# Kernel optimization log

Measured on AMD Instinct MI355X. Metric: run time of the kernel, lower is better.

The kernel has to match this reference:

```python
import jax, jax.numpy as jnp
import numpy as np

B, L, C = 4, 4096, 1024
NH, CS = 16, 16
HF = C // NH            # 64
NC = L // CS            # 256
LR = 1.0


def setup_inputs() -> dict:
    key = jax.random.key(0)
    ks = jax.random.split(key, 9)
    s = 0.02
    return {
        "hidden_states": jax.random.normal(ks[0], (B, L, C), jnp.float32),
        "Wq": jax.random.normal(ks[1], (C, C), jnp.float32) * s,
        "Wk": jax.random.normal(ks[2], (C, C), jnp.float32) * s,
        "Wv": jax.random.normal(ks[3], (C, C), jnp.float32) * s,
        "Wo": jax.random.normal(ks[4], (C, C), jnp.float32) * s,
        "ilr_w": jax.random.normal(ks[5], (C, NH), jnp.float32) * s,
        "ilr_b": jnp.zeros((NH,), jnp.float32),
        "W1": jax.random.normal(ks[6], (NH, HF, 4 * HF), jnp.float32) * s,
        "W2": jax.random.normal(ks[7], (NH, 4 * HF, HF), jnp.float32) * s,
    }


def _split(x):
    # [B,L,C] -> [B,NH,NC,CS,HF]
    return x.reshape(B, NC, CS, NH, HF).transpose(0, 3, 1, 2, 4)


def reference(hidden_states, Wq, Wk, Wv, Wo, ilr_w, ilr_b, W1, W2):
    XC = _split(hidden_states @ Wq)
    XB = _split(hidden_states @ Wk)
    XA = _split(hidden_states @ Wv)

    # inner-loop learning rate: [B,NH,NC,CS,1]
    ilr = jax.nn.sigmoid(hidden_states.reshape(B, NC, CS, C) @ ilr_w + ilr_b)
    ilr = ilr.transpose(0, 3, 1, 2)[..., None]
    token_idx = 1.0 / jnp.arange(1, CS + 1, dtype=jnp.float32)
    coeff = (LR * token_idx).reshape(1, 1, 1, CS, 1) * ilr / HF

    tril = jnp.tril(jnp.ones((CS, CS), hidden_states.dtype))

    # per-(batch,head) inner states
    W1s = jnp.broadcast_to(W1[None], (B, NH, HF, 4 * HF))
    W2s = jnp.broadcast_to(W2[None], (B, NH, 4 * HF, HF))

    def step(carry, xs):
        W1_s, W2_s = carry
        XA_c, XB_c, XC_c, coeff_c = xs          # [B,NH,CS,HF], coeff [B,NH,CS,1]
        coeff_last = coeff_c[..., -1:, :]        # [B,NH,1,1]
        Z1 = XB_c @ W1_s                         # [B,NH,CS,4HF]
        Z2 = Z1 @ W2_s                           # [B,NH,CS,HF]
        g2 = Z2 - XA_c
        g1 = g2 @ jnp.swapaxes(W2_s, -1, -2)
        Attn1 = tril * (XC_c @ jnp.swapaxes(XB_c, -1, -2))
        Z1_bar = XC_c @ W1_s - coeff_c * (Attn1 @ g1)
        W1_s = W1_s - jnp.swapaxes(coeff_last * XB_c, -1, -2) @ g1
        Attn2 = tril * (Z1_bar @ jnp.swapaxes(Z1, -1, -2))
        Z2_bar = Z1_bar @ W2_s - coeff_c * (Attn2 @ g2)
        W2_s = W2_s - jnp.swapaxes(coeff_last * Z1, -1, -2) @ g2
        return (W1_s, W2_s), Z2_bar

    # move chunk axis to front for scan: [NC,B,NH,CS,*]
    xs = tuple(t.transpose(2, 0, 1, 3, 4) for t in (XA, XB, XC, coeff))
    _, Z2_bars = jax.lax.scan(step, (W1s, W2s), xs)

    # [NC,B,NH,CS,HF] -> [B,NC,CS,NH,HF] -> [B,L,C]
    out = Z2_bars.transpose(1, 0, 3, 2, 4).reshape(B, L, C)
    return out @ Wo
```

## Files before the change

kernel.cpp:

```cpp
#include <hip/hip_runtime.h>

#define Bsz  4
#define Lsz  4096
#define Csz  1024
#define NHsz 16
#define CSsz 16
#define HFsz 64
#define HF4sz 256
#define NCsz 256

typedef __attribute__((ext_vector_type(8))) short  bhalf8;
typedef __attribute__((ext_vector_type(4))) float  floatx4;

__device__ __forceinline__ unsigned short bf_rne(float x) {
  const unsigned u = __float_as_uint(x);
  return (unsigned short)((u + 0x7fffu + ((u >> 16) & 1u)) >> 16);
}
__device__ __forceinline__ void split_rne(float x, unsigned short& h, unsigned short& l) {
  h = bf_rne(x);
  const float hf = __uint_as_float((unsigned)h << 16);
  l = bf_rne(x - hf);
}

__global__ __launch_bounds__(256)
void split32(const float* __restrict__ in, unsigned short* __restrict__ hi,
             unsigned short* __restrict__ lo)
{
  const int i = (blockIdx.x * 256 + threadIdx.x) * 4;
  const float4 v = *(const float4*)&in[i];
  ushort4 h, l;
  split_rne(v.x, h.x, l.x);
  split_rne(v.y, h.y, l.y);
  split_rne(v.z, h.z, l.z);
  split_rne(v.w, h.w, l.w);
  *(ushort4*)&hi[i] = h;
  *(ushort4*)&lo[i] = l;
}

__global__ __launch_bounds__(256)
void gemm_mfma(const unsigned short* __restrict__ Ahi,
               const unsigned short* __restrict__ Alo,
               const float* __restrict__ Bm,
               float* __restrict__ Cm, int M, int N, int K)
{
  __shared__ unsigned short sAh[128 * 40];
  __shared__ unsigned short sAl[128 * 40];
  __shared__ unsigned short sBh[128 * 40];
  __shared__ unsigned short sBl[128 * 40];

  const int t    = threadIdx.x;
  const int lane = t & 63, w = t >> 6;
  const int wr   = (w >> 1) * 64, wc = (w & 1) * 64;
  const int row0 = blockIdx.y * 128, col0 = blockIdx.x * 128;
  const int fr   = lane & 15, fk = (lane >> 4) * 8;

  floatx4 acc[4][4];
#pragma unroll
  for (int mi = 0; mi < 4; ++mi)
#pragma unroll
    for (int ni = 0; ni < 4; ++ni) acc[mi][ni] = (floatx4){0.f, 0.f, 0.f, 0.f};

  const int arow = t >> 1, akg = (t & 1) * 16;
  const int bc4  = (t & 31) * 4, bk4 = (t >> 5) * 4;

  for (int k0 = 0; k0 < K; k0 += 32) {
    {
      const size_t ga = (size_t)(row0 + arow) * K + k0 + akg;
      const bhalf8 h0 = *(const bhalf8*)&Ahi[ga];
      const bhalf8 h1 = *(const bhalf8*)&Ahi[ga + 8];
      const bhalf8 l0 = *(const bhalf8*)&Alo[ga];
      const bhalf8 l1 = *(const bhalf8*)&Alo[ga + 8];
      *(bhalf8*)&sAh[arow * 40 + akg]     = h0;
      *(bhalf8*)&sAh[arow * 40 + akg + 8] = h1;
      *(bhalf8*)&sAl[arow * 40 + akg]     = l0;
      *(bhalf8*)&sAl[arow * 40 + akg + 8] = l1;
    }
    {
      const float4 r0 = *(const float4*)&Bm[(size_t)(k0 + bk4 + 0) * N + col0 + bc4];
      const float4 r1 = *(const float4*)&Bm[(size_t)(k0 + bk4 + 1) * N + col0 + bc4];
      const float4 r2 = *(const float4*)&Bm[(size_t)(k0 + bk4 + 2) * N + col0 + bc4];
      const float4 r3 = *(const float4*)&Bm[(size_t)(k0 + bk4 + 3) * N + col0 + bc4];
#define STORE_BCOL(v0, v1, v2, v3, c) do {                                   \
      unsigned short h0_, h1_, h2_, h3_, l0_, l1_, l2_, l3_;                 \
      split_rne(v0, h0_, l0_); split_rne(v1, h1_, l1_);                      \
      split_rne(v2, h2_, l2_); split_rne(v3, h3_, l3_);                      \
      const int off_ = (bc4 + (c)) * 40 + bk4;                               \
      *(unsigned*)&sBh[off_]     = (unsigned)h0_ | ((unsigned)h1_ << 16);    \
      *(unsigned*)&sBh[off_ + 2] = (unsigned)h2_ | ((unsigned)h3_ << 16);    \
      *(unsigned*)&sBl[off_]     = (unsigned)l0_ | ((unsigned)l1_ << 16);    \
      *(unsigned*)&sBl[off_ + 2] = (unsigned)l2_ | ((unsigned)l3_ << 16);    \
    } while (0)
      STORE_BCOL(r0.x, r1.x, r2.x, r3.x, 0);
      STORE_BCOL(r0.y, r1.y, r2.y, r3.y, 1);
      STORE_BCOL(r0.z, r1.z, r2.z, r3.z, 2);
      STORE_BCOL(r0.w, r1.w, r2.w, r3.w, 3);
#undef STORE_BCOL
    }
    __syncthreads();

    bhalf8 ah[4], al[4];
#pragma unroll
    for (int mi = 0; mi < 4; ++mi) {
      ah[mi] = *(const bhalf8*)&sAh[(wr + mi * 16 + fr) * 40 + fk];
      al[mi] = *(const bhalf8*)&sAl[(wr + mi * 16 + fr) * 40 + fk];
    }
#pragma unroll
    for (int ni = 0; ni < 4; ++ni) {
      const bhalf8 bh = *(const bhalf8*)&sBh[(wc + ni * 16 + fr) * 40 + fk];
      const bhalf8 bl = *(const bhalf8*)&sBl[(wc + ni * 16 + fr) * 40 + fk];
#pragma unroll
      for (int mi = 0; mi < 4; ++mi) {
        acc[mi][ni] = __builtin_amdgcn_mfma_f32_16x16x32_bf16(ah[mi], bh, acc[mi][ni], 0, 0, 0);
        acc[mi][ni] = __builtin_amdgcn_mfma_f32_16x16x32_bf16(ah[mi], bl, acc[mi][ni], 0, 0, 0);
        acc[mi][ni] = __builtin_amdgcn_mfma_f32_16x16x32_bf16(al[mi], bh, acc[mi][ni], 0, 0, 0);
      }
    }
    __syncthreads();
  }

  const int er = (lane >> 4) * 4;
#pragma unroll
  for (int mi = 0; mi < 4; ++mi)
#pragma unroll
    for (int ni = 0; ni < 4; ++ni) {
      const size_t base = (size_t)(row0 + wr + mi * 16 + er) * N + col0 + wc + ni * 16 + fr;
#pragma unroll
      for (int j = 0; j < 4; ++j)
        Cm[base + (size_t)j * N] = acc[mi][ni][j];
    }
}

__global__ __launch_bounds__(256)
void ilr_coeff(const float* __restrict__ H, const float* __restrict__ Wil,
               const float* __restrict__ bil, float* __restrict__ coeff)
{
  __shared__ float sRow[4][1024];
  __shared__ float sP[4][16][17];
  const int t = threadIdx.x;
  const size_t r0 = (size_t)blockIdx.x * 4;
  for (int rr = 0; rr < 4; ++rr)
    for (int c = t; c < 1024; c += 256)
      sRow[rr][c] = H[(r0 + rr) * 1024 + c];
  __syncthreads();
  const int hh = t & 15, sl = t >> 4;
  for (int rr = 0; rr < 4; ++rr) {
    float acc = 0.f;
    for (int kk = 0; kk < 64; ++kk)
      acc += sRow[rr][sl * 64 + kk] * Wil[(sl * 64 + kk) * 16 + hh];
    sP[rr][sl][hh] = acc;
  }
  __syncthreads();
  if (t < 64) {
    const int rr = t >> 4, h2 = t & 15;
    float s = 0.f;
    for (int sl2 = 0; sl2 < 16; ++sl2) s += sP[rr][sl2][h2];
    s += bil[h2];
    const float sig = 1.f / (1.f + expf(-s));
    const int r  = (int)(r0 + rr);
    const int b  = r >> 12, l = r & 4095, nc = l >> 4, cs = l & 15;
    coeff[((b * 16 + h2) * NCsz + nc) * CSsz + cs] = sig / ((float)(cs + 1) * 64.0f);
  }
}

__global__ __launch_bounds__(512) __attribute__((amdgpu_waves_per_eu(1, 2)))
void ttt_scan(const float* __restrict__ XA, const float* __restrict__ XBuf,
              const float* __restrict__ XCbuf, const float* __restrict__ coeff,
              const float* __restrict__ W1g, const float* __restrict__ W2g,
              float* __restrict__ Out)
{
  __shared__ __attribute__((aligned(16))) float sg2[16 * 68];
  __shared__ __attribute__((aligned(16))) float sZ1[16 * 260];
  __shared__ __attribute__((aligned(16))) float sZ1b[16 * 260];
  __shared__ __attribute__((aligned(16))) float sTmp[10624];
  __shared__ float sA1[16 * 17];
  __shared__ float sA2[16 * 17];
  __shared__ float sCoBuf[2 * 16];

  const int t   = threadIdx.x;
  const int bh  = blockIdx.x;
  const int b   = bh >> 4, h = bh & 15;
  const bool isA = (t < 256);
  const int n   = t & 255;
  const int m   = t & 63, q = (t >> 6) & 3;

  float wreg[128];
#define W1R(k)  wreg[(k)]
#define ZBR(i)  wreg[64 + (i)]
#define G1R(i)  wreg[80 + (i)]
#define W2RR(k) wreg[(k)]
#define W2CR(k) wreg[64 + (k)]

  float xa0, xa1;

  const float* W1h = W1g + h * HFsz * HF4sz;
  const float* W2h = W2g + h * HF4sz * HFsz;
  if (isA) {
#pragma unroll
    for (int k = 0; k < 64; ++k) W1R(k) = W1h[k * 256 + n];
  } else {
#pragma unroll
    for (int mm = 0; mm < 64; ++mm) W2RR(mm) = W2h[n * 64 + mm];
#pragma unroll
    for (int kk = 0; kk < 64; ++kk) W2CR(kk) = W2h[(q * 64 + kk) * 64 + m];
  }

  {
    const int cb0 = (b * Lsz) * Csz + h * HFsz;
    if (t < 16) sCoBuf[t] = coeff[(bh * NCsz + 0) * CSsz + t];
    const int ibr = t >> 6, mm = t & 63;
    xa0 = XA[cb0 + ibr * 1024 + mm];
    xa1 = XA[cb0 + (ibr + 8) * 1024 + mm];
  }
  __syncthreads();

#pragma unroll 1
  for (int nc = 0; nc < NCsz; ++nc) {
    const int cur = nc & 1, nxt = cur ^ 1;
    const int cb  = (b * Lsz + nc * CSsz) * Csz + h * HFsz;
    const int nc1 = (nc + 1) & (NCsz - 1);
    const int cb1 = (b * Lsz + nc1 * CSsz) * Csz + h * HFsz;
    const float* __restrict__ xbG = XBuf  + cb;
    const float* __restrict__ xcG = XCbuf + cb;

    const float cl = sCoBuf[cur * 16 + 15];
    float conext = 0.f;
    if (isA && t < 16) conext = coeff[(bh * NCsz + nc1) * CSsz + t];

    if (isA) {
      float acc[16];
#pragma unroll
      for (int i = 0; i < 16; ++i) {
        float a0 = 0.f, a1 = 0.f;
#pragma unroll
        for (int k = 0; k < 64; k += 8) {
          const float4 x0 = *(const float4*)&xbG[i * 1024 + k];
          const float4 x1 = *(const float4*)&xbG[i * 1024 + k + 4];
          a0 = fmaf(x0.w, W1R(k + 3), fmaf(x0.z, W1R(k + 2),
               fmaf(x0.y, W1R(k + 1), fmaf(x0.x, W1R(k), a0))));
          a1 = fmaf(x1.w, W1R(k + 7), fmaf(x1.z, W1R(k + 6),
               fmaf(x1.y, W1R(k + 5), fmaf(x1.x, W1R(k + 4), a1))));
        }
        acc[i] = a0 + a1;
      }
#pragma unroll
      for (int i = 0; i < 16; ++i) sZ1[i * 260 + n] = acc[i];
    } else {
      const int ia = n >> 4, ja = n & 15;
      float a0 = 0.f, a1 = 0.f;
      if (ja <= ia) {
#pragma unroll
        for (int k = 0; k < 64; k += 8) {
          const float4 c0 = *(const float4*)&xcG[ia * 1024 + k];
          const float4 b0 = *(const float4*)&xbG[ja * 1024 + k];
          const float4 c1 = *(const float4*)&xcG[ia * 1024 + k + 4];
          const float4 b1 = *(const float4*)&xbG[ja * 1024 + k + 4];
          a0 = fmaf(c0.w, b0.w, fmaf(c0.z, b0.z, fmaf(c0.y, b0.y, fmaf(c0.x, b0.x, a0))));
          a1 = fmaf(c1.w, b1.w, fmaf(c1.z, b1.z, fmaf(c1.y, b1.y, fmaf(c1.x, b1.x, a1))));
        }
      }
      sA1[ia * 17 + ja] = a0 + a1;
    }
    __syncthreads();

    if (isA) {
#pragma unroll
      for (int i = 0; i < 16; ++i) {
        float a0 = 0.f, a1 = 0.f;
#pragma unroll
        for (int k = 0; k < 64; k += 8) {
          const float4 x0 = *(const float4*)&xcG[i * 1024 + k];
          const float4 x1 = *(const float4*)&xcG[i * 1024 + k + 4];
          a0 = fmaf(x0.w, W1R(k + 3), fmaf(x0.z, W1R(k + 2),
               fmaf(x0.y, W1R(k + 1), fmaf(x0.x, W1R(k), a0))));
          a1 = fmaf(x1.w, W1R(k + 7), fmaf(x1.z, W1R(k + 6),
               fmaf(x1.y, W1R(k + 5), fmaf(x1.x, W1R(k + 4), a1))));
        }
        ZBR(i) = a0 + a1;
      }
    } else {
      const int qo = q << 6;
      float acc[16];
#pragma unroll
      for (int i = 0; i < 16; ++i) acc[i] = 0.f;
#pragma unroll
      for (int kk = 0; kk < 64; kk += 4) {
        const float wa = W2CR(kk), wb = W2CR(kk + 1), wc = W2CR(kk + 2), wd = W2CR(kk + 3);
#pragma unroll
        for (int i = 0; i < 16; ++i) {
          const float4 z = *(const float4*)&sZ1[i * 260 + qo + kk];
          acc[i] = fmaf(z.w, wd, fmaf(z.z, wc, fmaf(z.y, wb, fmaf(z.x, wa, acc[i]))));
        }
      }
#pragma unroll
      for (int i = 0; i < 16; ++i) sTmp[(q << 10) + (i << 6) + m] = acc[i];
    }
    __syncthreads();

    {
      const int ibr = t >> 6, mm = t & 63;
      const int i1 = ibr + 8;
      float v0 = sTmp[ibr * 64 + mm] + sTmp[1024 + ibr * 64 + mm]
               + sTmp[2048 + ibr * 64 + mm] + sTmp[3072 + ibr * 64 + mm] - xa0;
      float v1 = sTmp[i1 * 64 + mm] + sTmp[1024 + i1 * 64 + mm]
               + sTmp[2048 + i1 * 64 + mm] + sTmp[3072 + i1 * 64 + mm] - xa1;
      sg2[ibr * 68 + mm] = v0;
      sg2[i1 * 68 + mm]  = v1;
      xa0 = XA[cb1 + ibr * 1024 + mm];
      xa1 = XA[cb1 + i1 * 1024 + mm];
      if (t < 16) sCoBuf[nxt * 16 + t] = conext;
    }
    __syncthreads();

    if (!isA) {
      float s[16];
#pragma unroll
      for (int i = 0; i < 16; ++i) s[i] = cl * sZ1[i * 260 + n];
      float acc[16];
#pragma unroll
      for (int i = 0; i < 16; ++i) acc[i] = 0.f;
#pragma unroll
      for (int mm = 0; mm < 64; mm += 4) {
        const float wa = W2RR(mm), wb = W2RR(mm + 1), wc = W2RR(mm + 2), wd = W2RR(mm + 3);
        float d0 = 0.f, d1 = 0.f, d2 = 0.f, d3 = 0.f;
#pragma unroll
        for (int i = 0; i < 16; ++i) {
          const float4 g = *(const float4*)&sg2[i * 68 + mm];
          acc[i] = fmaf(g.w, wd, fmaf(g.z, wc, fmaf(g.y, wb, fmaf(g.x, wa, acc[i]))));
          d0 = fmaf(s[i], g.x, d0); d1 = fmaf(s[i], g.y, d1);
          d2 = fmaf(s[i], g.z, d2); d3 = fmaf(s[i], g.w, d3);
        }
        W2RR(mm + 0) -= d0; W2RR(mm + 1) -= d1; W2RR(mm + 2) -= d2; W2RR(mm + 3) -= d3;
      }
#pragma unroll
      for (int i = 0; i < 16; ++i) sTmp[i * 256 + n] = acc[i];
    }
    __syncthreads();

    if (isA) {
#pragma unroll
      for (int j = 0; j < 16; ++j) G1R(j) = sTmp[j * 256 + n];
#pragma unroll
      for (int i = 0; i < 16; ++i) {
        float at = 0.f;
#pragma unroll
        for (int j = 0; j <= i; ++j) at = fmaf(sA1[i * 17 + j], G1R(j), at);
        ZBR(i) = fmaf(-sCoBuf[cur * 16 + i], at, ZBR(i));
        sZ1b[i * 260 + n] = ZBR(i);
      }
    }
    __syncthreads();

    if (isA) {
      const int ia = n >> 4, ja = n & 15;
      float a0 = 0.f, a1 = 0.f, a2 = 0.f, a3 = 0.f;
      if (ja <= ia) {
#pragma unroll
        for (int kk = 0; kk < 256; kk += 16) {
          const float4 p0 = *(const float4*)&sZ1b[ia * 260 + kk];
          const float4 z0 = *(const float4*)&sZ1 [ja * 260 + kk];
          const float4 p1 = *(const float4*)&sZ1b[ia * 260 + kk + 4];
          const float4 z1 = *(const float4*)&sZ1 [ja * 260 + kk + 4];
          const float4 p2 = *(const float4*)&sZ1b[ia * 260 + kk + 8];
          const float4 z2 = *(const float4*)&sZ1 [ja * 260 + kk + 8];
          const float4 p3 = *(const float4*)&sZ1b[ia * 260 + kk + 12];
          const float4 z3 = *(const float4*)&sZ1 [ja * 260 + kk + 12];
          a0 = fmaf(p0.w, z0.w, fmaf(p0.z, z0.z, fmaf(p0.y, z0.y, fmaf(p0.x, z0.x, a0))));
          a1 = fmaf(p1.w, z1.w, fmaf(p1.z, z1.z, fmaf(p1.y, z1.y, fmaf(p1.x, z1.x, a1))));
          a2 = fmaf(p2.w, z2.w, fmaf(p2.z, z2.z, fmaf(p2.y, z2.y, fmaf(p2.x, z2.x, a2))));
          a3 = fmaf(p3.w, z3.w, fmaf(p3.z, z3.z, fmaf(p3.y, z3.y, fmaf(p3.x, z3.x, a3))));
        }
      }
      sA2[ia * 17 + ja] = (a0 + a1) + (a2 + a3);
#pragma unroll
      for (int i = 0; i < 16; ++i) {
        const float gi = cl * G1R(i);
#pragma unroll
        for (int k = 0; k < 64; k += 4) {
          const float4 x = *(const float4*)&xbG[i * 1024 + k];
          W1R(k + 0) -= gi * x.x; W1R(k + 1) -= gi * x.y;
          W1R(k + 2) -= gi * x.z; W1R(k + 3) -= gi * x.w;
        }
      }
    } else {
      const int qo = q << 6;
      float acc[16];
#pragma unroll
      for (int i = 0; i < 16; ++i) acc[i] = 0.f;
#pragma unroll
      for (int kk = 0; kk < 64; kk += 4) {
        const float wa = W2CR(kk), wb = W2CR(kk + 1), wc = W2CR(kk + 2), wd = W2CR(kk + 3);
#pragma unroll
        for (int i = 0; i < 16; ++i) {
          const float4 z = *(const float4*)&sZ1b[i * 260 + qo + kk];
          acc[i] = fmaf(z.w, wd, fmaf(z.z, wc, fmaf(z.y, wb, fmaf(z.x, wa, acc[i]))));
        }
      }
#pragma unroll
      for (int i = 0; i < 16; ++i) sTmp[(q << 10) + (i << 6) + m] = acc[i];
      float s2[16];
#pragma unroll
      for (int i = 0; i < 16; ++i) s2[i] = cl * sg2[i * 68 + m];
#pragma unroll
      for (int kk = 0; kk < 64; kk += 4) {
        float d0 = 0.f, d1 = 0.f, d2 = 0.f, d3 = 0.f;
#pragma unroll
        for (int i = 0; i < 16; ++i) {
          const float4 z = *(const float4*)&sZ1[i * 260 + qo + kk];
          d0 = fmaf(s2[i], z.x, d0); d1 = fmaf(s2[i], z.y, d1);
          d2 = fmaf(s2[i], z.z, d2); d3 = fmaf(s2[i], z.w, d3);
        }
        W2CR(kk + 0) -= d0; W2CR(kk + 1) -= d1; W2CR(kk + 2) -= d2; W2CR(kk + 3) -= d3;
      }
    }
    __syncthreads();

    if (isA) {
      const int q4 = n >> 6, mm = n & 63;
#pragma unroll
      for (int r = 0; r < 4; ++r) {
        const int i = q4 + 4 * r;
        float v = sTmp[i * 64 + mm] + sTmp[1024 + i * 64 + mm]
                + sTmp[2048 + i * 64 + mm] + sTmp[3072 + i * 64 + mm];
        float at = 0.f;
#pragma unroll
        for (int j = 0; j < 16; ++j) at = fmaf(sA2[i * 17 + j], sg2[j * 68 + mm], at);
        Out[cb + i * 1024 + mm] = v - sCoBuf[cur * 16 + i] * at;
      }
    }
  }
#undef W1R
#undef ZBR
#undef G1R
#undef W2RR
#undef W2CR
}

extern "C" void kernel_launch(void* const* d_in, const int* in_sizes, int n_in,
                              void* d_out, int out_size, void* d_ws, size_t ws_size,
                              hipStream_t stream)
{
  const float* H    = (const float*)d_in[0];
  const float* Wq   = (const float*)d_in[1];
  const float* Wk   = (const float*)d_in[2];
  const float* Wv   = (const float*)d_in[3];
  const float* Wo   = (const float*)d_in[4];
  const float* Wil  = (const float*)d_in[5];
  const float* bil  = (const float*)d_in[6];
  const float* W1   = (const float*)d_in[7];
  const float* W2   = (const float*)d_in[8];
  float* out        = (float*)d_out;

  float* ws    = (float*)d_ws;
  float* bXC   = ws;
  float* bXB   = ws + 16777216;
  float* bZ2b  = ws + 33554432;
  float* bCo   = ws + 50331648;
  float* bXA   = out;

  unsigned short* hHi = (unsigned short*)bZ2b;
  unsigned short* hLo = hHi + 16777216;
  unsigned short* zHi = (unsigned short*)bXC;
  unsigned short* zLo = zHi + 16777216;

  const int M = Bsz * Lsz, N = Csz, K = Csz;
  dim3 gm(N / 128, M / 128);
  dim3 bm(256);

  split32<<<16384, 256, 0, stream>>>(H, hHi, hLo);
  gemm_mfma<<<gm, bm, 0, stream>>>(hHi, hLo, Wq, bXC, M, N, K);
  gemm_mfma<<<gm, bm, 0, stream>>>(hHi, hLo, Wk, bXB, M, N, K);
  gemm_mfma<<<gm, bm, 0, stream>>>(hHi, hLo, Wv, bXA, M, N, K);
  ilr_coeff<<<M / 4, 256, 0, stream>>>(H, Wil, bil, bCo);
  ttt_scan<<<Bsz * NHsz, 512, 0, stream>>>(bXA, bXB, bXC, bCo, W1, W2, bZ2b);
  split32<<<16384, 256, 0, stream>>>(bZ2b, zHi, zLo);
  gemm_mfma<<<gm, bm, 0, stream>>>(zHi, zLo, Wo, out, M, N, K);
}
```

Measured before the change: 9.513 ms.

## Move TTT scan chunk matmuls onto bf16x3 MFMA with split-precision fragments

Rewrites the per-chunk inner loop of the sequential TTT scan so the Z1, XC·W1, Z2, g1, Z2_bar and Attn2 products run on 16x16x32 bf16 MFMA instructions. Each fp32 operand is split into hi/lo bf16 parts and three MFMAs per tile approximate fp32 accuracy. Register and shared-memory layouts are reorganised around MFMA fragments: W2 is mirrored into shared memory as hi/lo bf16, transposed copies of Z1, G1 and XB support the weight updates, and the pipeline gains extra barriers. The scalar FMA work and LDS traffic of the old VALU path should shrink, at the cost of split/convert overhead, a slightly different numerical result, and more synchronisation steps per chunk.

```diff
diff --git a/kernel.cpp b/kernel.cpp
--- a/kernel.cpp
+++ b/kernel.cpp
@@ -21,6 +21,29 @@
   const float hf = __uint_as_float((unsigned)h << 16);
   l = bf_rne(x - hf);
 }
+__device__ __forceinline__ void tsplit(float x, unsigned short& h, unsigned short& l) {
+  const unsigned u = __float_as_uint(x);
+  h = (unsigned short)(u >> 16);
+  const float r = x - __uint_as_float(u & 0xffff0000u);
+  l = bf_rne(r);
+}
+__device__ __forceinline__ void split_frag8(const float* __restrict__ x,
+                                            bhalf8& h, bhalf8& l) {
+#pragma unroll
+  for (int e = 0; e < 8; ++e) {
+    unsigned short hs, ls;
+    tsplit(x[e], hs, ls);
+    h[e] = (short)hs; l[e] = (short)ls;
+  }
+}
+__device__ __forceinline__ float recon2(unsigned short h, unsigned short l) {
+  return __uint_as_float((unsigned)h << 16) + __uint_as_float((unsigned)l << 16);
+}
+
+#define MFMA3(acc, ah, al, bh, bl)                                            \
+  acc = __builtin_amdgcn_mfma_f32_16x16x32_bf16(ah, bh, acc, 0, 0, 0);        \
+  acc = __builtin_amdgcn_mfma_f32_16x16x32_bf16(ah, bl, acc, 0, 0, 0);        \
+  acc = __builtin_amdgcn_mfma_f32_16x16x32_bf16(al, bh, acc, 0, 0, 0);
 
 __global__ __launch_bounds__(256)
 void split32(const float* __restrict__ in, unsigned short* __restrict__ hi,
@@ -162,90 +185,138 @@
   }
 }
 
-__global__ __launch_bounds__(512) __attribute__((amdgpu_waves_per_eu(1, 2)))
+__global__ __launch_bounds__(512)
 void ttt_scan(const float* __restrict__ XA, const float* __restrict__ XBuf,
               const float* __restrict__ XCbuf, const float* __restrict__ coeff,
               const float* __restrict__ W1g, const float* __restrict__ W2g,
               float* __restrict__ Out)
 {
-  __shared__ __attribute__((aligned(16))) float sg2[16 * 68];
-  __shared__ __attribute__((aligned(16))) float sZ1[16 * 260];
-  __shared__ __attribute__((aligned(16))) float sZ1b[16 * 260];
-  __shared__ __attribute__((aligned(16))) float sTmp[10624];
-  __shared__ float sA1[16 * 17];
-  __shared__ float sA2[16 * 17];
-  __shared__ float sCoBuf[2 * 16];
-
-  const int t   = threadIdx.x;
-  const int bh  = blockIdx.x;
-  const int b   = bh >> 4, h = bh & 15;
-  const bool isA = (t < 256);
-  const int n   = t & 255;
-  const int m   = t & 63, q = (t >> 6) & 3;
-
-  float wreg[128];
-#define W1R(k)  wreg[(k)]
-#define ZBR(i)  wreg[64 + (i)]
-#define G1R(i)  wreg[80 + (i)]
-#define W2RR(k) wreg[(k)]
-#define W2CR(k) wreg[64 + (k)]
-
-  float xa0, xa1;
+  __shared__ __attribute__((aligned(16))) unsigned short sW2h[256 * 72];
+  __shared__ __attribute__((aligned(16))) unsigned short sW2l[256 * 72];
+  __shared__ __attribute__((aligned(16))) unsigned short sZ1h[16 * 264];
+  __shared__ __attribute__((aligned(16))) unsigned short sZ1l[16 * 264];
+  __shared__ __attribute__((aligned(16))) unsigned short sZbh[16 * 264];
+  __shared__ __attribute__((aligned(16))) unsigned short sZbl[16 * 264];
+  __shared__ __attribute__((aligned(16))) float sZ1t[256 * 20];
+  __shared__ __attribute__((aligned(16))) float sG1 [256 * 20];
+  __shared__ __attribute__((aligned(16))) unsigned short sg2h[16 * 72];
+  __shared__ __attribute__((aligned(16))) unsigned short sg2l[16 * 72];
+  __shared__ __attribute__((aligned(16))) float sXBt[64 * 20];
+  __shared__ __attribute__((aligned(16))) float sA1 [16 * 17];
+  __shared__ __attribute__((aligned(16))) float sA2p[4 * 16 * 17];
+  __shared__ __attribute__((aligned(16))) float sCo [2 * 16];
+
+  const int t    = threadIdx.x;
+  const int bh   = blockIdx.x;
+  const int b    = bh >> 4, h = bh & 15;
+  const bool isA = (t < 512 / 2);
+  const int lane = t & 63;
+  const int fr   = lane & 15, fg = lane >> 4;
+  const int w    = t >> 6;
+  const int tb   = t - 256;
+  const int wb   = (t >> 6) & 3;
+  const int m    = 16 * wb + fr;
+
+  float w1m[64];
+  float w2m[64];
+  floatx4 zba[4];
+  floatx4 zb2;
+  float xar[4];
 
   const float* W1h = W1g + h * HFsz * HF4sz;
   const float* W2h = W2g + h * HF4sz * HFsz;
   if (isA) {
 #pragma unroll
-    for (int k = 0; k < 64; ++k) W1R(k) = W1h[k * 256 + n];
+    for (int tt = 0; tt < 4; ++tt)
+#pragma unroll
+      for (int ks = 0; ks < 2; ++ks)
+#pragma unroll
+        for (int e = 0; e < 8; ++e)
+          w1m[tt * 16 + ks * 8 + e] = W1h[(32 * ks + 8 * fg + e) * 256 + (64 * w + 16 * tt + fr)];
   } else {
 #pragma unroll
-    for (int mm = 0; mm < 64; ++mm) W2RR(mm) = W2h[n * 64 + mm];
-#pragma unroll
-    for (int kk = 0; kk < 64; ++kk) W2CR(kk) = W2h[(q * 64 + kk) * 64 + m];
-  }
-
-  {
+    for (int ks = 0; ks < 8; ++ks)
+#pragma unroll
+      for (int e = 0; e < 8; ++e)
+        w2m[ks * 8 + e] = W2h[(32 * ks + 8 * fg + e) * 64 + m];
+#pragma unroll
+    for (int ks = 0; ks < 8; ++ks)
+#pragma unroll
+      for (int e = 0; e < 8; ++e) {
+        const int k = 32 * ks + 8 * fg + e;
+        unsigned short hs, ls;
+        tsplit(w2m[ks * 8 + e], hs, ls);
+        sW2h[k * 72 + m] = hs;
+        sW2l[k * 72 + m] = ls;
+      }
     const int cb0 = (b * Lsz) * Csz + h * HFsz;
-    if (t < 16) sCoBuf[t] = coeff[(bh * NCsz + 0) * CSsz + t];
-    const int ibr = t >> 6, mm = t & 63;
-    xa0 = XA[cb0 + ibr * 1024 + mm];
-    xa1 = XA[cb0 + (ibr + 8) * 1024 + mm];
+#pragma unroll
+    for (int j = 0; j < 4; ++j)
+      xar[j] = XA[cb0 + (4 * fg + j) * 1024 + m];
   }
   __syncthreads();
 
 #pragma unroll 1
   for (int nc = 0; nc < NCsz; ++nc) {
-    const int cur = nc & 1, nxt = cur ^ 1;
+    const int cur = nc & 1;
     const int cb  = (b * Lsz + nc * CSsz) * Csz + h * HFsz;
     const int nc1 = (nc + 1) & (NCsz - 1);
     const int cb1 = (b * Lsz + nc1 * CSsz) * Csz + h * HFsz;
     const float* __restrict__ xbG = XBuf  + cb;
     const float* __restrict__ xcG = XCbuf + cb;
 
-    const float cl = sCoBuf[cur * 16 + 15];
-    float conext = 0.f;
-    if (isA && t < 16) conext = coeff[(bh * NCsz + nc1) * CSsz + t];
-
     if (isA) {
-      float acc[16];
-#pragma unroll
-      for (int i = 0; i < 16; ++i) {
-        float a0 = 0.f, a1 = 0.f;
-#pragma unroll
-        for (int k = 0; k < 64; k += 8) {
-          const float4 x0 = *(const float4*)&xbG[i * 1024 + k];
-          const float4 x1 = *(const float4*)&xbG[i * 1024 + k + 4];
-          a0 = fmaf(x0.w, W1R(k + 3), fmaf(x0.z, W1R(k + 2),
-               fmaf(x0.y, W1R(k + 1), fmaf(x0.x, W1R(k), a0))));
-          a1 = fmaf(x1.w, W1R(k + 7), fmaf(x1.z, W1R(k + 6),
-               fmaf(x1.y, W1R(k + 5), fmaf(x1.x, W1R(k + 4), a1))));
-        }
-        acc[i] = a0 + a1;
-      }
-#pragma unroll
-      for (int i = 0; i < 16; ++i) sZ1[i * 260 + n] = acc[i];
+      if (t < 16) sCo[cur * 16 + t] = coeff[(bh * NCsz + nc) * CSsz + t];
+      const float* __restrict__ xbp = xbG + fr * 1024 + 8 * fg;
+      const float* __restrict__ xcp = xcG + fr * 1024 + 8 * fg;
+      {
+        floatx4 acc[4];
+#pragma unroll
+        for (int tt = 0; tt < 4; ++tt) acc[tt] = (floatx4){0.f, 0.f, 0.f, 0.f};
+#pragma unroll
+        for (int ks = 0; ks < 2; ++ks) {
+          float xv[8];
+          *(float4*)&xv[0] = *(const float4*)&xbp[32 * ks];
+          *(float4*)&xv[4] = *(const float4*)&xbp[32 * ks + 4];
+          bhalf8 xh, xl; split_frag8(xv, xh, xl);
+#pragma unroll
+          for (int tt = 0; tt < 4; ++tt) {
+            bhalf8 wh, wl; split_frag8(&w1m[tt * 16 + ks * 8], wh, wl);
+            MFMA3(acc[tt], xh, xl, wh, wl);
+          }
+        }
+#pragma unroll
+        for (int tt = 0; tt < 4; ++tt) {
+          const int n = 64 * w + 16 * tt + fr;
+#pragma unroll
+          for (int j = 0; j < 4; ++j) {
+            const int i = 4 * fg + j;
+            const float v = acc[tt][j];
+            unsigned short hs, ls; tsplit(v, hs, ls);
+            sZ1h[i * 264 + n] = hs;
+            sZ1l[i * 264 + n] = ls;
+            sZ1t[n * 20 + i]  = v;
+          }
+        }
+      }
+      {
+#pragma unroll
+        for (int tt = 0; tt < 4; ++tt) zba[tt] = (floatx4){0.f, 0.f, 0.f, 0.f};
+#pragma unroll
+        for (int ks = 0; ks < 2; ++ks) {
+          float xv[8];
+          *(float4*)&xv[0] = *(const float4*)&xcp[32 * ks];
+          *(float4*)&xv[4] = *(const float4*)&xcp[32 * ks + 4];
+          bhalf8 xh, xl; split_frag8(xv, xh, xl);
+#pragma unroll
+          for (int tt = 0; tt < 4; ++tt) {
+            bhalf8 wh, wl; split_frag8(&w1m[tt * 16 + ks * 8], wh, wl);
+            MFMA3(zba[tt], xh, xl, wh, wl);
+          }
+        }
+      }
     } else {
-      const int ia = n >> 4, ja = n & 15;
+      const int ia = tb >> 4, ja = tb & 15;
       float a0 = 0.f, a1 = 0.f;
       if (ja <= ia) {
 #pragma unroll
@@ -262,177 +333,182 @@
     }
     __syncthreads();
 
+    if (!isA) {
+      floatx4 z2a = (floatx4){0.f, 0.f, 0.f, 0.f};
+#pragma unroll
+      for (int ks = 0; ks < 8; ++ks) {
+        const bhalf8 ah = *(const bhalf8*)&sZ1h[fr * 264 + 32 * ks + 8 * fg];
+        const bhalf8 al = *(const bhalf8*)&sZ1l[fr * 264 + 32 * ks + 8 * fg];
+        bhalf8 wh, wl; split_frag8(&w2m[ks * 8], wh, wl);
+        MFMA3(z2a, ah, al, wh, wl);
+      }
+#pragma unroll
+      for (int j = 0; j < 4; ++j) {
+        const int i = 4 * fg + j;
+        const float g2v = z2a[j] - xar[j];
+        unsigned short hs, ls; tsplit(g2v, hs, ls);
+        sg2h[i * 72 + m] = hs;
+        sg2l[i * 72 + m] = ls;
+      }
+    } else {
+      const int ir = t >> 4, k4 = (t & 15) * 4;
+      const float4 v = *(const float4*)&xbG[ir * 1024 + k4];
+      sXBt[(k4 + 0) * 20 + ir] = v.x;
+      sXBt[(k4 + 1) * 20 + ir] = v.y;
+      sXBt[(k4 + 2) * 20 + ir] = v.z;
+      sXBt[(k4 + 3) * 20 + ir] = v.w;
+    }
+    __syncthreads();
+
+    if (!isA) {
+      floatx4 g1a[4];
+#pragma unroll
+      for (int r = 0; r < 4; ++r) g1a[r] = (floatx4){0.f, 0.f, 0.f, 0.f};
+#pragma unroll
+      for (int ks2 = 0; ks2 < 2; ++ks2) {
+        const bhalf8 gh = *(const bhalf8*)&sg2h[fr * 72 + 32 * ks2 + 8 * fg];
+        const bhalf8 gl = *(const bhalf8*)&sg2l[fr * 72 + 32 * ks2 + 8 * fg];
+#pragma unroll
+        for (int r = 0; r < 4; ++r) {
+          const int rt = 4 * wb + r;
+          const bhalf8 ah = *(const bhalf8*)&sW2h[(16 * rt + fr) * 72 + 32 * ks2 + 8 * fg];
+          const bhalf8 al = *(const bhalf8*)&sW2l[(16 * rt + fr) * 72 + 32 * ks2 + 8 * fg];
+          MFMA3(g1a[r], ah, al, gh, gl);
+        }
+      }
+#pragma unroll
+      for (int r = 0; r < 4; ++r) {
+        const int rt = 4 * wb + r;
+#pragma unroll
+        for (int j = 0; j < 4; ++j)
+          sG1[(16 * rt + 4 * fg + j) * 20 + fr] = g1a[r][j];
+      }
+    }
+    __syncthreads();
+
     if (isA) {
 #pragma unroll
+      for (int tt = 0; tt < 4; ++tt) {
+        const int n = 64 * w + 16 * tt + fr;
+        float gv[16];
+        *(float4*)&gv[0]  = *(const float4*)&sG1[n * 20 + 0];
+        *(float4*)&gv[4]  = *(const float4*)&sG1[n * 20 + 4];
+        *(float4*)&gv[8]  = *(const float4*)&sG1[n * 20 + 8];
+        *(float4*)&gv[12] = *(const float4*)&sG1[n * 20 + 12];
+#pragma unroll
+        for (int j = 0; j < 4; ++j) {
+          const int i = 4 * fg + j;
+          float at = 0.f;
+#pragma unroll
+          for (int jp = 0; jp < 16; ++jp)
+            at = fmaf(sA1[i * 17 + jp], gv[jp], at);
+          const float z = zba[tt][j] - sCo[cur * 16 + i] * at;
+          unsigned short hs, ls; tsplit(z, hs, ls);
+          sZbh[i * 264 + n] = hs;
+          sZbl[i * 264 + n] = ls;
+        }
+      }
+    }
+    __syncthreads();
+
+    if (isA) {
+      floatx4 a2 = (floatx4){0.f, 0.f, 0.f, 0.f};
+#pragma unroll
+      for (int ksl = 0; ksl < 2; ++ksl) {
+        const int ks = 2 * w + ksl;
+        const bhalf8 ah = *(const bhalf8*)&sZbh[fr * 264 + 32 * ks + 8 * fg];
+        const bhalf8 al = *(const bhalf8*)&sZbl[fr * 264 + 32 * ks + 8 * fg];
+        const bhalf8 bhf = *(const bhalf8*)&sZ1h[fr * 264 + 32 * ks + 8 * fg];
+        const bhalf8 blf = *(const bhalf8*)&sZ1l[fr * 264 + 32 * ks + 8 * fg];
+        MFMA3(a2, ah, al, bhf, blf);
+      }
+#pragma unroll
+      for (int j = 0; j < 4; ++j) {
+        const int i = 4 * fg + j;
+        sA2p[w * 272 + i * 17 + fr] = (fr <= i) ? a2[j] : 0.f;
+      }
+      const float cl = sCo[cur * 16 + 15];
+#pragma unroll
       for (int i = 0; i < 16; ++i) {
-        float a0 = 0.f, a1 = 0.f;
-#pragma unroll
-        for (int k = 0; k < 64; k += 8) {
-          const float4 x0 = *(const float4*)&xcG[i * 1024 + k];
-          const float4 x1 = *(const float4*)&xcG[i * 1024 + k + 4];
-          a0 = fmaf(x0.w, W1R(k + 3), fmaf(x0.z, W1R(k + 2),
-               fmaf(x0.y, W1R(k + 1), fmaf(x0.x, W1R(k), a0))));
-          a1 = fmaf(x1.w, W1R(k + 7), fmaf(x1.z, W1R(k + 6),
-               fmaf(x1.y, W1R(k + 5), fmaf(x1.x, W1R(k + 4), a1))));
-        }
-        ZBR(i) = a0 + a1;
+        float cg[4];
+#pragma unroll
+        for (int tt = 0; tt < 4; ++tt)
+          cg[tt] = cl * sG1[(64 * w + 16 * tt + fr) * 20 + i];
+#pragma unroll
+        for (int ks = 0; ks < 2; ++ks)
+#pragma unroll
+          for (int e = 0; e < 8; ++e) {
+            const float xb = sXBt[(32 * ks + 8 * fg + e) * 20 + i];
+#pragma unroll
+            for (int tt = 0; tt < 4; ++tt)
+              w1m[tt * 16 + ks * 8 + e] = fmaf(-cg[tt], xb, w1m[tt * 16 + ks * 8 + e]);
+          }
       }
     } else {
-      const int qo = q << 6;
-      float acc[16];
-#pragma unroll
-      for (int i = 0; i < 16; ++i) acc[i] = 0.f;
-#pragma unroll
-      for (int kk = 0; kk < 64; kk += 4) {
-        const float wa = W2CR(kk), wb = W2CR(kk + 1), wc = W2CR(kk + 2), wd = W2CR(kk + 3);
-#pragma unroll
-        for (int i = 0; i < 16; ++i) {
-          const float4 z = *(const float4*)&sZ1[i * 260 + qo + kk];
-          acc[i] = fmaf(z.w, wd, fmaf(z.z, wc, fmaf(z.y, wb, fmaf(z.x, wa, acc[i]))));
-        }
-      }
-#pragma unroll
-      for (int i = 0; i < 16; ++i) sTmp[(q << 10) + (i << 6) + m] = acc[i];
-    }
-    __syncthreads();
-
-    {
-      const int ibr = t >> 6, mm = t & 63;
-      const int i1 = ibr + 8;
-      float v0 = sTmp[ibr * 64 + mm] + sTmp[1024 + ibr * 64 + mm]
-               + sTmp[2048 + ibr * 64 + mm] + sTmp[3072 + ibr * 64 + mm] - xa0;
-      float v1 = sTmp[i1 * 64 + mm] + sTmp[1024 + i1 * 64 + mm]
-               + sTmp[2048 + i1 * 64 + mm] + sTmp[3072 + i1 * 64 + mm] - xa1;
-      sg2[ibr * 68 + mm] = v0;
-      sg2[i1 * 68 + mm]  = v1;
-      xa0 = XA[cb1 + ibr * 1024 + mm];
-      xa1 = XA[cb1 + i1 * 1024 + mm];
-      if (t < 16) sCoBuf[nxt * 16 + t] = conext;
+      zb2 = (floatx4){0.f, 0.f, 0.f, 0.f};
+#pragma unroll
+      for (int ks = 0; ks < 8; ++ks) {
+        const bhalf8 ah = *(const bhalf8*)&sZbh[fr * 264 + 32 * ks + 8 * fg];
+        const bhalf8 al = *(const bhalf8*)&sZbl[fr * 264 + 32 * ks + 8 * fg];
+        bhalf8 wh, wl; split_frag8(&w2m[ks * 8], wh, wl);
+        MFMA3(zb2, ah, al, wh, wl);
+      }
+      const float cl = sCo[cur * 16 + 15];
+      float cg[16];
+#pragma unroll
+      for (int i = 0; i < 16; ++i)
+        cg[i] = cl * recon2(sg2h[i * 72 + m], sg2l[i * 72 + m]);
+#pragma unroll
+      for (int ks = 0; ks < 8; ++ks)
+#pragma unroll
+        for (int e = 0; e < 8; ++e) {
+          const int k = 32 * ks + 8 * fg + e;
+          float zr[16];
+          *(float4*)&zr[0]  = *(const float4*)&sZ1t[k * 20 + 0];
+          *(float4*)&zr[4]  = *(const float4*)&sZ1t[k * 20 + 4];
+          *(float4*)&zr[8]  = *(const float4*)&sZ1t[k * 20 + 8];
+          *(float4*)&zr[12] = *(const float4*)&sZ1t[k * 20 + 12];
+          float acc = w2m[ks * 8 + e];
+#pragma unroll
+          for (int i = 0; i < 16; ++i) acc = fmaf(-cg[i], zr[i], acc);
+          w2m[ks * 8 + e] = acc;
+        }
     }
     __syncthreads();
 
     if (!isA) {
-      float s[16];
-#pragma unroll
-      for (int i = 0; i < 16; ++i) s[i] = cl * sZ1[i * 260 + n];
-      float acc[16];
-#pragma unroll
-      for (int i = 0; i < 16; ++i) acc[i] = 0.f;
-#pragma unroll
-      for (int mm = 0; mm < 64; mm += 4) {
-        const float wa = W2RR(mm), wb = W2RR(mm + 1), wc = W2RR(mm + 2), wd = W2RR(mm + 3);
-        float d0 = 0.f, d1 = 0.f, d2 = 0.f, d3 = 0.f;
-#pragma unroll
-        for (int i = 0; i < 16; ++i) {
-          const float4 g = *(const float4*)&sg2[i * 68 + mm];
-          acc[i] = fmaf(g.w, wd, fmaf(g.z, wc, fmaf(g.y, wb, fmaf(g.x, wa, acc[i]))));
-          d0 = fmaf(s[i], g.x, d0); d1 = fmaf(s[i], g.y, d1);
-          d2 = fmaf(s[i], g.z, d2); d3 = fmaf(s[i], g.w, d3);
-        }
-        W2RR(mm + 0) -= d0; W2RR(mm + 1) -= d1; W2RR(mm + 2) -= d2; W2RR(mm + 3) -= d3;
-      }
-#pragma unroll
-      for (int i = 0; i < 16; ++i) sTmp[i * 256 + n] = acc[i];
-    }
-    __syncthreads();
-
-    if (isA) {
-#pragma unroll
-      for (int j = 0; j < 16; ++j) G1R(j) = sTmp[j * 256 + n];
-#pragma unroll
-      for (int i = 0; i < 16; ++i) {
-        float at = 0.f;
-#pragma unroll
-        for (int j = 0; j <= i; ++j) at = fmaf(sA1[i * 17 + j], G1R(j), at);
-        ZBR(i) = fmaf(-sCoBuf[cur * 16 + i], at, ZBR(i));
-        sZ1b[i * 260 + n] = ZBR(i);
-      }
-    }
-    __syncthreads();
-
-    if (isA) {
-      const int ia = n >> 4, ja = n & 15;
-      float a0 = 0.f, a1 = 0.f, a2 = 0.f, a3 = 0.f;
-      if (ja <= ia) {
-#pragma unroll
-        for (int kk = 0; kk < 256; kk += 16) {
-          const float4 p0 = *(const float4*)&sZ1b[ia * 260 + kk];
-          const float4 z0 = *(const float4*)&sZ1 [ja * 260 + kk];
-          const float4 p1 = *(const float4*)&sZ1b[ia * 260 + kk + 4];
-          const float4 z1 = *(const float4*)&sZ1 [ja * 260 + kk + 4];
-          const float4 p2 = *(const float4*)&sZ1b[ia * 260 + kk + 8];
-          const float4 z2 = *(const float4*)&sZ1 [ja * 260 + kk + 8];
-          const float4 p3 = *(const float4*)&sZ1b[ia * 260 + kk + 12];
-          const float4 z3 = *(const float4*)&sZ1 [ja * 260 + kk + 12];
-          a0 = fmaf(p0.w, z0.w, fmaf(p0.z, z0.z, fmaf(p0.y, z0.y, fmaf(p0.x, z0.x, a0))));
-          a1 = fmaf(p1.w, z1.w, fmaf(p1.z, z1.z, fmaf(p1.y, z1.y, fmaf(p1.x, z1.x, a1))));
-          a2 = fmaf(p2.w, z2.w, fmaf(p2.z, z2.z, fmaf(p2.y, z2.y, fmaf(p2.x, z2.x, a2))));
-          a3 = fmaf(p3.w, z3.w, fmaf(p3.z, z3.z, fmaf(p3.y, z3.y, fmaf(p3.x, z3.x, a3))));
-        }
-      }
-      sA2[ia * 17 + ja] = (a0 + a1) + (a2 + a3);
-#pragma unroll
-      for (int i = 0; i < 16; ++i) {
-        const float gi = cl * G1R(i);
-#pragma unroll
-        for (int k = 0; k < 64; k += 4) {
-          const float4 x = *(const float4*)&xbG[i * 1024 + k];
-          W1R(k + 0) -= gi * x.x; W1R(k + 1) -= gi * x.y;
-          W1R(k + 2) -= gi * x.z; W1R(k + 3) -= gi * x.w;
-        }
-      }
-    } else {
-      const int qo = q << 6;
-      float acc[16];
-#pragma unroll
-      for (int i = 0; i < 16; ++i) acc[i] = 0.f;
-#pragma unroll
-      for (int kk = 0; kk < 64; kk += 4) {
-        const float wa = W2CR(kk), wb = W2CR(kk + 1), wc = W2CR(kk + 2), wd = W2CR(kk + 3);
-#pragma unroll
-        for (int i = 0; i < 16; ++i) {
-          const float4 z = *(const float4*)&sZ1b[i * 260 + qo + kk];
-          acc[i] = fmaf(z.w, wd, fmaf(z.z, wc, fmaf(z.y, wb, fmaf(z.x, wa, acc[i]))));
-        }
-      }
-#pragma unroll
-      for (int i = 0; i < 16; ++i) sTmp[(q << 10) + (i << 6) + m] = acc[i];
-      float s2[16];
-#pragma unroll
-      for (int i = 0; i < 16; ++i) s2[i] = cl * sg2[i * 68 + m];
-#pragma unroll
-      for (int kk = 0; kk < 64; kk += 4) {
-        float d0 = 0.f, d1 = 0.f, d2 = 0.f, d3 = 0.f;
-#pragma unroll
-        for (int i = 0; i < 16; ++i) {
-          const float4 z = *(const float4*)&sZ1[i * 260 + qo + kk];
-          d0 = fmaf(s2[i], z.x, d0); d1 = fmaf(s2[i], z.y, d1);
-          d2 = fmaf(s2[i], z.z, d2); d3 = fmaf(s2[i], z.w, d3);
-        }
-        W2CR(kk + 0) -= d0; W2CR(kk + 1) -= d1; W2CR(kk + 2) -= d2; W2CR(kk + 3) -= d3;
-      }
-    }
-    __syncthreads();
-
-    if (isA) {
-      const int q4 = n >> 6, mm = n & 63;
-#pragma unroll
-      for (int r = 0; r < 4; ++r) {
-        const int i = q4 + 4 * r;
-        float v = sTmp[i * 64 + mm] + sTmp[1024 + i * 64 + mm]
-                + sTmp[2048 + i * 64 + mm] + sTmp[3072 + i * 64 + mm];
-        float at = 0.f;
-#pragma unroll
-        for (int j = 0; j < 16; ++j) at = fmaf(sA2[i * 17 + j], sg2[j * 68 + mm], at);
-        Out[cb + i * 1024 + mm] = v - sCoBuf[cur * 16 + i] * at;
-      }
+      float at[4] = {0.f, 0.f, 0.f, 0.f};
+#pragma unroll
+      for (int jp = 0; jp < 16; ++jp) {
+        const float g2v = recon2(sg2h[jp * 72 + m], sg2l[jp * 72 + m]);
+#pragma unroll
+        for (int j = 0; j < 4; ++j) {
+          const int i = 4 * fg + j;
+          const float a2s = sA2p[i * 17 + jp] + sA2p[272 + i * 17 + jp]
+                          + sA2p[544 + i * 17 + jp] + sA2p[816 + i * 17 + jp];
+          at[j] = fmaf(a2s, g2v, at[j]);
+        }
+      }
+#pragma unroll
+      for (int j = 0; j < 4; ++j) {
+        const int i = 4 * fg + j;
+        Out[cb + i * 1024 + m] = zb2[j] - sCo[cur * 16 + i] * at[j];
+      }
+#pragma unroll
+      for (int ks = 0; ks < 8; ++ks)
+#pragma unroll
+        for (int e = 0; e < 8; ++e) {
+          const int k = 32 * ks + 8 * fg + e;
+          unsigned short hs, ls;
+          tsplit(w2m[ks * 8 + e], hs, ls);
+          sW2h[k * 72 + m] = hs;
+          sW2l[k * 72 + m] = ls;
+        }
+#pragma unroll
+      for (int j = 0; j < 4; ++j)
+        xar[j] = XA[cb1 + (4 * fg + j) * 1024 + m];
     }
   }
-#undef W1R
-#undef ZBR
-#undef G1R
-#undef W2RR
-#undef W2CR
 }
 
 extern "C" void kernel_launch(void* const* d_in, const int* in_sizes, int n_in,
```

Result: faster. 8.694 ms (-8.6%).
